# Kernel optimization log

Hardware: AMD Instinct MI355X
Metric: run time of the kernel (lower is better)

Reference implementation:

```python
import jax, jax.numpy as jnp
import numpy as np

B, S, E, L = 4, 4096, 64, 3
INIT_SCALE = 0.03


def setup_inputs() -> dict:
    key = jax.random.key(0)
    ks = jax.random.split(key, 7)
    return {
        "x": jax.random.normal(ks[0], (B, S, S + 1), dtype=jnp.float32),
        "q_ws": jax.random.normal(ks[1], (L, E, E), dtype=jnp.float32) * INIT_SCALE,
        "k_ws": jax.random.normal(ks[2], (L, E, E), dtype=jnp.float32) * INIT_SCALE,
        "v_ws": jax.random.normal(ks[3], (L, E, E), dtype=jnp.float32) * INIT_SCALE,
        "random_matrix": jax.random.normal(ks[4], (S, E - 1), dtype=jnp.float32) * INIT_SCALE,
        "coeffs_attended": jax.random.normal(ks[5], (S, E), dtype=jnp.float32) * INIT_SCALE,
        "offset": jax.random.normal(ks[6], (1,), dtype=jnp.float32),
    }


def reference(x, q_ws, k_ws, v_ws, random_matrix, coeffs_attended, offset):
    seq_length = random_matrix.shape[0]
    # project first seq_length feature columns, keep the last column raw -> [B, S, E]
    av = jnp.concatenate(
        [jnp.einsum('bsf,fe->bse', x[:, :, :seq_length], random_matrix), x[:, :, -1:]],
        axis=2,
    )

    def layer(av, ws):
        qw, kw, vw = ws
        q = jnp.einsum('bse,ed->bsd', av, qw)   # [B, S, E]
        k = jnp.einsum('bse,ed->bsd', av, kw)
        v = jnp.einsum('bse,ed->bsd', av, vw)
        scores = jax.nn.softmax(jnp.einsum('bqd,bkd->bqk', q, k), axis=-1)  # [B, S, S]
        out = jnp.einsum('bqk,bkd->bqd', scores, v)
        # skip_connections=False: output replaces attended values
        return out, None

    av, _ = jax.lax.scan(layer, av, (q_ws, k_ws, v_ws))
    final = jnp.einsum('bij,ij->b', av, coeffs_attended)  # [B]
    return final + offset[0]
```

## Files before the change

### kernel.cpp

```cpp
#include <hip/hip_runtime.h>

#define SEQ  4096
#define EMB  64
#define NB   4
#define XROW 4097

#define SW(r, c) ((r) * 64 + (((c) ^ ((r) & 7)) << 3))

typedef unsigned short ushort_t;
typedef __attribute__((ext_vector_type(8))) short short8;
typedef __attribute__((ext_vector_type(4))) float floatx4;

union U8 { uint4 u; short8 s8; };

__device__ __forceinline__ ushort_t f2bf(float f) {
    union { float f; unsigned int u; } v; v.f = f;
    unsigned int r = v.u + 0x7FFFu + ((v.u >> 16) & 1u);
    return (ushort_t)(r >> 16);
}
__device__ __forceinline__ uint2 pack4bf(float a, float b, float c, float d) {
    uint2 p;
    p.x = (unsigned)f2bf(a) | ((unsigned)f2bf(b) << 16);
    p.y = (unsigned)f2bf(c) | ((unsigned)f2bf(d) << 16);
    return p;
}

__global__ __launch_bounds__(256) void prep_rmt(const float* __restrict__ rm,
                                                ushort_t* __restrict__ rmT,
                                                float* __restrict__ out,
                                                const float* __restrict__ offset) {
    if (blockIdx.x == 0 && threadIdx.x < NB) out[threadIdx.x] = offset[0];
    int o = (blockIdx.x * 256 + threadIdx.x) * 4;
    int e = o >> 12;
    int f = o & 4095;
    alignas(8) ushort_t t[4];
    t[0] = f2bf((e < 63) ? rm[(size_t)(f + 0) * 63 + e] : 0.f);
    t[1] = f2bf((e < 63) ? rm[(size_t)(f + 1) * 63 + e] : 0.f);
    t[2] = f2bf((e < 63) ? rm[(size_t)(f + 2) * 63 + e] : 0.f);
    t[3] = f2bf((e < 63) ? rm[(size_t)(f + 3) * 63 + e] : 0.f);
    *(uint2*)&rmT[o] = *(uint2*)t;
}

__global__ __launch_bounds__(512) void proj_mfma(const float* __restrict__ x,
        const ushort_t* __restrict__ rmT, float* __restrict__ av) {
    __shared__ ushort_t xs[2][64 * 64];
    __shared__ ushort_t rs[2][64 * 64];
    const int tid = threadIdx.x;
    const int row0 = blockIdx.x * 64;
    const int w = tid >> 6, l = tid & 63;
    const int wg = w >> 2;
    const int wq = w & 3;
    const int t4 = tid & 255;
    const int srow = t4 >> 2, sc = (t4 & 3) * 16;
    const int c0 = (t4 & 3) * 2;
    const int kbase = wg * 2048;
    const int quad = l >> 4, q16 = l & 15;

    floatx4 acc[4];
    #pragma unroll
    for (int i = 0; i < 4; ++i) acc[i] = (floatx4){0.f, 0.f, 0.f, 0.f};

    float px[16];
    short8 pr0, pr1;
    {
        const float* xp = x + (size_t)(row0 + srow) * XROW + kbase + sc;
        #pragma unroll
        for (int i = 0; i < 16; ++i) px[i] = xp[i];
        const ushort_t* rp = rmT + (size_t)srow * SEQ + kbase + sc;
        pr0 = *(const short8*)&rp[0];
        pr1 = *(const short8*)&rp[8];
    }

    for (int k0 = 0; k0 < 2048; k0 += 64) {
        __syncthreads();
        {
            alignas(16) ushort_t tmp[16];
            #pragma unroll
            for (int i = 0; i < 16; ++i) tmp[i] = f2bf(px[i]);
            *(short8*)&xs[wg][SW(srow, c0)]     = *(short8*)&tmp[0];
            *(short8*)&xs[wg][SW(srow, c0 + 1)] = *(short8*)&tmp[8];
            *(short8*)&rs[wg][SW(srow, c0)]     = pr0;
            *(short8*)&rs[wg][SW(srow, c0 + 1)] = pr1;
        }
        __syncthreads();
        if (k0 + 64 < 2048) {
            const float* xp = x + (size_t)(row0 + srow) * XROW + kbase + k0 + 64 + sc;
            #pragma unroll
            for (int i = 0; i < 16; ++i) px[i] = xp[i];
            const ushort_t* rp = rmT + (size_t)srow * SEQ + kbase + k0 + 64 + sc;
            pr0 = *(const short8*)&rp[0];
            pr1 = *(const short8*)&rp[8];
        }
        #pragma unroll
        for (int ksp = 0; ksp < 2; ++ksp) {
            short8 a = *(short8*)&xs[wg][SW(wq * 16 + q16, ksp * 4 + quad)];
            #pragma unroll
            for (int nt = 0; nt < 4; ++nt) {
                short8 bf = *(short8*)&rs[wg][SW(nt * 16 + q16, ksp * 4 + quad)];
                acc[nt] = __builtin_amdgcn_mfma_f32_16x16x32_bf16(a, bf, acc[nt], 0, 0, 0);
            }
        }
    }

    __syncthreads();
    float* poc = (float*)xs;
    if (wg == 1) {
        #pragma unroll
        for (int nt = 0; nt < 4; ++nt)
            #pragma unroll
            for (int r = 0; r < 4; ++r)
                poc[(wq * 16 + quad * 4 + r) * 64 + nt * 16 + q16] = acc[nt][r];
    }
    __syncthreads();
    if (wg == 0) {
        #pragma unroll
        for (int nt = 0; nt < 4; ++nt)
            #pragma unroll
            for (int r = 0; r < 4; ++r) {
                int row = row0 + wq * 16 + quad * 4 + r;
                int col = nt * 16 + q16;
                float v = acc[nt][r] + poc[(wq * 16 + quad * 4 + r) * 64 + col];
                if (col == 63) v = x[(size_t)row * XROW + SEQ];
                av[(size_t)row * EMB + col] = v;
            }
    }
}

__global__ __launch_bounds__(256) void qkv_mfma(const float* __restrict__ av,
        const float* __restrict__ qw, const float* __restrict__ kw,
        const float* __restrict__ vw, ushort_t* __restrict__ Qb,
        ushort_t* __restrict__ Kb, ushort_t* __restrict__ Vt) {
    __shared__ ushort_t avs[64 * 64];
    __shared__ ushort_t wqs[64 * 64], wks[64 * 64], wvs[64 * 64];
    const int tid = threadIdx.x;
    const int row0 = blockIdx.x * 64;
    const int w = tid >> 6, l = tid & 63;
    const int srow = tid >> 2, sc = (tid & 3) * 16;
    const int c0 = (tid & 3) * 2;

    {
        const float* ap = av + (size_t)(row0 + srow) * EMB + sc;
        alignas(16) ushort_t tmp[16];
        #pragma unroll
        for (int i = 0; i < 16; ++i) tmp[i] = f2bf(ap[i]);
        *(short8*)&avs[SW(srow, c0)]     = *(short8*)&tmp[0];
        *(short8*)&avs[SW(srow, c0 + 1)] = *(short8*)&tmp[8];
    }
    {
        alignas(16) ushort_t tq[16], tk[16], tv[16];
        #pragma unroll
        for (int i = 0; i < 16; ++i) {
            int kk = sc + i;
            tq[i] = f2bf(qw[kk * 64 + srow]);
            tk[i] = f2bf(kw[kk * 64 + srow]);
            tv[i] = f2bf(vw[kk * 64 + srow]);
        }
        *(short8*)&wqs[SW(srow, c0)]     = *(short8*)&tq[0];
        *(short8*)&wqs[SW(srow, c0 + 1)] = *(short8*)&tq[8];
        *(short8*)&wks[SW(srow, c0)]     = *(short8*)&tk[0];
        *(short8*)&wks[SW(srow, c0 + 1)] = *(short8*)&tk[8];
        *(short8*)&wvs[SW(srow, c0)]     = *(short8*)&tv[0];
        *(short8*)&wvs[SW(srow, c0 + 1)] = *(short8*)&tv[8];
    }
    __syncthreads();

    floatx4 aq[4], ak[4], avv[4];
    #pragma unroll
    for (int i = 0; i < 4; ++i) {
        aq[i] = (floatx4){0.f, 0.f, 0.f, 0.f};
        ak[i] = aq[i]; avv[i] = aq[i];
    }
    #pragma unroll
    for (int ksp = 0; ksp < 2; ++ksp) {
        short8 a = *(short8*)&avs[SW(w * 16 + (l & 15), ksp * 4 + (l >> 4))];
        #pragma unroll
        for (int nt = 0; nt < 4; ++nt) {
            int bo = SW(nt * 16 + (l & 15), ksp * 4 + (l >> 4));
            aq[nt]  = __builtin_amdgcn_mfma_f32_16x16x32_bf16(a, *(short8*)&wqs[bo], aq[nt], 0, 0, 0);
            ak[nt]  = __builtin_amdgcn_mfma_f32_16x16x32_bf16(a, *(short8*)&wks[bo], ak[nt], 0, 0, 0);
            avv[nt] = __builtin_amdgcn_mfma_f32_16x16x32_bf16(a, *(short8*)&wvs[bo], avv[nt], 0, 0, 0);
        }
    }

    const int b = row0 >> 12;
    #pragma unroll
    for (int nt = 0; nt < 4; ++nt)
        #pragma unroll
        for (int r = 0; r < 4; ++r) {
            int row = row0 + w * 16 + (l >> 4) * 4 + r;
            int col = nt * 16 + (l & 15);
            size_t o = (size_t)row * EMB + col;
            Qb[o] = f2bf(aq[nt][r]);
            Kb[o] = f2bf(ak[nt][r]);
            Vt[((size_t)b * EMB + col) * SEQ + (row & 4095)] = f2bf(avv[nt][r]);
        }
}

__global__ __launch_bounds__(512) void flash_mfma(const ushort_t* __restrict__ Qb,
        const ushort_t* __restrict__ Kb, const ushort_t* __restrict__ Vt,
        float* __restrict__ out) {
    __shared__ ushort_t ks[2][64 * 64];
    __shared__ ushort_t vt[2][64 * 64];
    __shared__ ushort_t psbuf[8 * 1024];
    __shared__ float lrow[2][64];
    const int tid = threadIdx.x;
    const int w = tid >> 6, l = tid & 63;
    const int wg = w >> 2, wq = w & 3;
    const int quad = l >> 4, q16 = l & 15;
    const int b = blockIdx.y;
    const int q0 = blockIdx.x * 64;
    const size_t base  = (size_t)b * SEQ * EMB;
    const size_t vbase = (size_t)b * EMB * SEQ;
    const int t4 = tid & 255;
    const int srow = t4 >> 2, sc = (t4 & 3) * 16;
    const int c0 = (t4 & 3) * 2;
    const int kbase = wg * 2048;
    ushort_t* ps = &psbuf[w * 1024];

    short8 qf[2];
    #pragma unroll
    for (int ksp = 0; ksp < 2; ++ksp)
        qf[ksp] = *(const short8*)&Qb[base + (size_t)(q0 + wq * 16 + q16) * EMB
                                      + ksp * 32 + quad * 8];

    short8 pk0, pk1, pv0, pv1;
    {
        const ushort_t* kp = Kb + base + (size_t)(kbase + srow) * EMB + sc;
        pk0 = *(const short8*)kp;
        pk1 = *(const short8*)(kp + 8);
        const ushort_t* vp = Vt + vbase + (size_t)srow * SEQ + kbase + sc;
        pv0 = *(const short8*)vp;
        pv1 = *(const short8*)(vp + 8);
    }

    floatx4 o_acc[4];
    #pragma unroll
    for (int i = 0; i < 4; ++i) o_acc[i] = (floatx4){0.f, 0.f, 0.f, 0.f};
    float lpart = 0.f;

    for (int kt0 = 0; kt0 < 2048; kt0 += 64) {
        __syncthreads();
        *(short8*)&ks[wg][SW(srow, c0)]     = pk0;
        *(short8*)&ks[wg][SW(srow, c0 + 1)] = pk1;
        *(short8*)&vt[wg][SW(srow, c0)]     = pv0;
        *(short8*)&vt[wg][SW(srow, c0 + 1)] = pv1;
        __syncthreads();
        if (kt0 + 64 < 2048) {
            const ushort_t* kp = Kb + base + (size_t)(kbase + kt0 + 64 + srow) * EMB + sc;
            pk0 = *(const short8*)kp;
            pk1 = *(const short8*)(kp + 8);
            const ushort_t* vp = Vt + vbase + (size_t)srow * SEQ + kbase + kt0 + 64 + sc;
            pv0 = *(const short8*)vp;
            pv1 = *(const short8*)(vp + 8);
        }

        floatx4 s[4];
        #pragma unroll
        for (int nt = 0; nt < 4; ++nt) s[nt] = (floatx4){0.f, 0.f, 0.f, 0.f};
        #pragma unroll
        for (int ksp = 0; ksp < 2; ++ksp)
            #pragma unroll
            for (int nt = 0; nt < 4; ++nt) {
                short8 a = *(short8*)&ks[wg][SW(nt * 16 + q16, ksp * 4 + quad)];
                s[nt] = __builtin_amdgcn_mfma_f32_16x16x32_bf16(a, qf[ksp], s[nt], 0, 0, 0);
            }

        #pragma unroll
        for (int nt = 0; nt < 4; ++nt) {
            float p0 = __expf(s[nt][0]);
            float p1 = __expf(s[nt][1]);
            float p2 = __expf(s[nt][2]);
            float p3 = __expf(s[nt][3]);
            lpart += (p0 + p1) + (p2 + p3);
            int g = nt * 4 + quad;
            *(uint2*)&ps[q16 * 64 + ((g ^ q16) & 15) * 4] = pack4bf(p0, p1, p2, p3);
        }
        asm volatile("s_waitcnt lgkmcnt(0)" ::: "memory");

        #pragma unroll
        for (int ksp = 0; ksp < 2; ++ksp) {
            int g0 = ksp * 8 + quad * 2;
            uint2 a0 = *(uint2*)&ps[q16 * 64 + ((g0 ^ q16) & 15) * 4];
            uint2 a1 = *(uint2*)&ps[q16 * 64 + (((g0 + 1) ^ q16) & 15) * 4];
            U8 af;
            af.u.x = a0.x; af.u.y = a0.y; af.u.z = a1.x; af.u.w = a1.y;
            #pragma unroll
            for (int nt = 0; nt < 4; ++nt) {
                short8 bf = *(short8*)&vt[wg][SW(nt * 16 + q16, ksp * 4 + quad)];
                o_acc[nt] = __builtin_amdgcn_mfma_f32_16x16x32_bf16(af.s8, bf, o_acc[nt], 0, 0, 0);
            }
        }
    }

    lpart += __shfl_xor(lpart, 16);
    lpart += __shfl_xor(lpart, 32);
    __syncthreads();
    if (quad == 0) lrow[wg][wq * 16 + q16] = lpart;
    float* oc = (float*)psbuf;
    if (wg == 1) {
        #pragma unroll
        for (int nt = 0; nt < 4; ++nt)
            #pragma unroll
            for (int r = 0; r < 4; ++r)
                oc[(wq * 16 + quad * 4 + r) * 64 + nt * 16 + q16] = o_acc[nt][r];
    }
    __syncthreads();
    if (wg == 0) {
        float linv[4];
        #pragma unroll
        for (int r = 0; r < 4; ++r) {
            int q = wq * 16 + quad * 4 + r;
            linv[r] = 1.f / (lrow[0][q] + lrow[1][q]);
        }
        #pragma unroll
        for (int nt = 0; nt < 4; ++nt)
            #pragma unroll
            for (int r = 0; r < 4; ++r) {
                int row = q0 + wq * 16 + quad * 4 + r;
                int col = nt * 16 + q16;
                float v = (o_acc[nt][r] + oc[(wq * 16 + quad * 4 + r) * 64 + col]) * linv[r];
                out[base + (size_t)row * EMB + col] = v;
            }
    }
}

__global__ __launch_bounds__(256) void reduce_kernel(const float* __restrict__ av,
        const float* __restrict__ coeffs, float* __restrict__ out) {
    const int b = blockIdx.y;
    const size_t base = (size_t)b * SEQ * EMB;
    const int local0 = blockIdx.x * 4096;
    const int tid = threadIdx.x;
    float ssum = 0.f;
    #pragma unroll
    for (int i = 0; i < 4; ++i) {
        int idx = local0 + (tid + i * 256) * 4;
        float4 a = *(const float4*)&av[base + idx];
        float4 c = *(const float4*)&coeffs[idx];
        ssum += a.x * c.x + a.y * c.y + a.z * c.z + a.w * c.w;
    }
    #pragma unroll
    for (int off = 1; off < 64; off <<= 1) ssum += __shfl_xor(ssum, off);
    __shared__ float wsum[4];
    if ((tid & 63) == 0) wsum[tid >> 6] = ssum;
    __syncthreads();
    if (tid == 0)
        atomicAdd(&out[b], wsum[0] + wsum[1] + wsum[2] + wsum[3]);
}

extern "C" void kernel_launch(void* const* d_in, const int* in_sizes, int n_in,
                              void* d_out, int out_size, void* d_ws, size_t ws_size,
                              hipStream_t stream) {
    const float* x      = (const float*)d_in[0];
    const float* q_ws   = (const float*)d_in[1];
    const float* k_ws   = (const float*)d_in[2];
    const float* v_ws   = (const float*)d_in[3];
    const float* rm     = (const float*)d_in[4];
    const float* coeffs = (const float*)d_in[5];
    const float* offset = (const float*)d_in[6];
    float* out = (float*)d_out;
    char* ws = (char*)d_ws;

    float*    AV  = (float*)ws;
    ushort_t* Qb  = (ushort_t*)(ws + 4 * 1024 * 1024);
    ushort_t* Kb  = (ushort_t*)(ws + 6 * 1024 * 1024);
    ushort_t* Vt  = (ushort_t*)(ws + 8 * 1024 * 1024);
    ushort_t* rmT = (ushort_t*)(ws + 10 * 1024 * 1024);

    prep_rmt<<<256, 256, 0, stream>>>(rm, rmT, out, offset);
    proj_mfma<<<256, 512, 0, stream>>>(x, rmT, AV);
    for (int layer = 0; layer < 3; ++layer) {
        qkv_mfma<<<256, 256, 0, stream>>>(AV, q_ws + layer * 4096,
                                          k_ws + layer * 4096, v_ws + layer * 4096,
                                          Qb, Kb, Vt);
        flash_mfma<<<dim3(64, NB), 512, 0, stream>>>(Qb, Kb, Vt, AV);
    }
    reduce_kernel<<<dim3(64, NB), 256, 0, stream>>>(AV, coeffs, out);
}
```

Before: 531.8 us.

## Restructure flash kernel: 4-way key split, 32 query rows per wave, direct global K/V loads

The flash attention kernel now splits keys four ways across wave groups instead of two, and each wave handles 32 query rows so every K fragment feeds two MFMAs. K and V fragments are read straight from global memory (L2) into registers, which removes the shared-memory staging and the barriers inside the loop. A remapped block index spreads batches across XCDs. The cost is more global traffic per wave, higher register pressure, and a larger shared-memory reduction of four partial outputs at the end.

New measurement: 593.8 us. 11.7% more time.

```diff
diff --git a/kernel.cpp b/kernel.cpp
--- a/kernel.cpp
+++ b/kernel.cpp
@@ -199,128 +199,144 @@
 __global__ __launch_bounds__(512) void flash_mfma(const ushort_t* __restrict__ Qb,
         const ushort_t* __restrict__ Kb, const ushort_t* __restrict__ Vt,
         float* __restrict__ out) {
-    __shared__ ushort_t ks[2][64 * 64];
-    __shared__ ushort_t vt[2][64 * 64];
-    __shared__ ushort_t psbuf[8 * 1024];
-    __shared__ float lrow[2][64];
+    __shared__ ushort_t psbuf[8 * 2048];
+    __shared__ float comb[3][64 * 64];
+    __shared__ float lrow[4][64];
     const int tid = threadIdx.x;
     const int w = tid >> 6, l = tid & 63;
-    const int wg = w >> 2, wq = w & 3;
+    const int wg = w >> 1;
+    const int wq = w & 1;
     const int quad = l >> 4, q16 = l & 15;
-    const int b = blockIdx.y;
-    const int q0 = blockIdx.x * 64;
+    const int id2 = (blockIdx.x & 7) * 32 + (blockIdx.x >> 3);
+    const int b = id2 >> 6;
+    const int q0 = (id2 & 63) * 64;
     const size_t base  = (size_t)b * SEQ * EMB;
     const size_t vbase = (size_t)b * EMB * SEQ;
-    const int t4 = tid & 255;
-    const int srow = t4 >> 2, sc = (t4 & 3) * 16;
-    const int c0 = (t4 & 3) * 2;
-    const int kbase = wg * 2048;
-    ushort_t* ps = &psbuf[w * 1024];
-
-    short8 qf[2];
-    #pragma unroll
-    for (int ksp = 0; ksp < 2; ++ksp)
-        qf[ksp] = *(const short8*)&Qb[base + (size_t)(q0 + wq * 16 + q16) * EMB
-                                      + ksp * 32 + quad * 8];
-
-    short8 pk0, pk1, pv0, pv1;
-    {
-        const ushort_t* kp = Kb + base + (size_t)(kbase + srow) * EMB + sc;
-        pk0 = *(const short8*)kp;
-        pk1 = *(const short8*)(kp + 8);
-        const ushort_t* vp = Vt + vbase + (size_t)srow * SEQ + kbase + sc;
-        pv0 = *(const short8*)vp;
-        pv1 = *(const short8*)(vp + 8);
-    }
-
-    floatx4 o_acc[4];
-    #pragma unroll
-    for (int i = 0; i < 4; ++i) o_acc[i] = (floatx4){0.f, 0.f, 0.f, 0.f};
-    float lpart = 0.f;
-
-    for (int kt0 = 0; kt0 < 2048; kt0 += 64) {
-        __syncthreads();
-        *(short8*)&ks[wg][SW(srow, c0)]     = pk0;
-        *(short8*)&ks[wg][SW(srow, c0 + 1)] = pk1;
-        *(short8*)&vt[wg][SW(srow, c0)]     = pv0;
-        *(short8*)&vt[wg][SW(srow, c0 + 1)] = pv1;
-        __syncthreads();
-        if (kt0 + 64 < 2048) {
-            const ushort_t* kp = Kb + base + (size_t)(kbase + kt0 + 64 + srow) * EMB + sc;
-            pk0 = *(const short8*)kp;
-            pk1 = *(const short8*)(kp + 8);
-            const ushort_t* vp = Vt + vbase + (size_t)srow * SEQ + kbase + kt0 + 64 + sc;
-            pv0 = *(const short8*)vp;
-            pv1 = *(const short8*)(vp + 8);
-        }
-
-        floatx4 s[4];
-        #pragma unroll
-        for (int nt = 0; nt < 4; ++nt) s[nt] = (floatx4){0.f, 0.f, 0.f, 0.f};
+    const int kbase = wg * 1024;
+    ushort_t* ps = &psbuf[w * 2048];
+
+    short8 qf[2][2];
+    #pragma unroll
+    for (int qh = 0; qh < 2; ++qh)
         #pragma unroll
         for (int ksp = 0; ksp < 2; ++ksp)
+            qf[qh][ksp] = *(const short8*)&Qb[base
+                + (size_t)(q0 + wq * 32 + qh * 16 + q16) * EMB + ksp * 32 + quad * 8];
+
+    floatx4 o_acc[2][4];
+    #pragma unroll
+    for (int qh = 0; qh < 2; ++qh)
+        #pragma unroll
+        for (int i = 0; i < 4; ++i) o_acc[qh][i] = (floatx4){0.f, 0.f, 0.f, 0.f};
+    float lp0 = 0.f, lp1 = 0.f;
+
+    for (int kt0 = 0; kt0 < 1024; kt0 += 64) {
+        const int kt = kbase + kt0;
+
+        floatx4 s[2][4];
+        #pragma unroll
+        for (int qh = 0; qh < 2; ++qh)
+            #pragma unroll
+            for (int nt = 0; nt < 4; ++nt) s[qh][nt] = (floatx4){0.f, 0.f, 0.f, 0.f};
+        #pragma unroll
+        for (int ksp = 0; ksp < 2; ++ksp) {
+            short8 akf[4];
+            #pragma unroll
+            for (int nt = 0; nt < 4; ++nt)
+                akf[nt] = *(const short8*)&Kb[base
+                    + (size_t)(kt + nt * 16 + q16) * EMB + ksp * 32 + quad * 8];
             #pragma unroll
             for (int nt = 0; nt < 4; ++nt) {
-                short8 a = *(short8*)&ks[wg][SW(nt * 16 + q16, ksp * 4 + quad)];
-                s[nt] = __builtin_amdgcn_mfma_f32_16x16x32_bf16(a, qf[ksp], s[nt], 0, 0, 0);
-            }
+                s[0][nt] = __builtin_amdgcn_mfma_f32_16x16x32_bf16(akf[nt], qf[0][ksp], s[0][nt], 0, 0, 0);
+                s[1][nt] = __builtin_amdgcn_mfma_f32_16x16x32_bf16(akf[nt], qf[1][ksp], s[1][nt], 0, 0, 0);
+            }
+        }
+
+        short8 bv[2][4];
+        #pragma unroll
+        for (int ksp = 0; ksp < 2; ++ksp)
+            #pragma unroll
+            for (int nt = 0; nt < 4; ++nt)
+                bv[ksp][nt] = *(const short8*)&Vt[vbase
+                    + (size_t)(nt * 16 + q16) * SEQ + kt + ksp * 32 + quad * 8];
 
         #pragma unroll
         for (int nt = 0; nt < 4; ++nt) {
-            float p0 = __expf(s[nt][0]);
-            float p1 = __expf(s[nt][1]);
-            float p2 = __expf(s[nt][2]);
-            float p3 = __expf(s[nt][3]);
-            lpart += (p0 + p1) + (p2 + p3);
+            float p0 = __expf(s[0][nt][0]);
+            float p1 = __expf(s[0][nt][1]);
+            float p2 = __expf(s[0][nt][2]);
+            float p3 = __expf(s[0][nt][3]);
+            lp0 += (p0 + p1) + (p2 + p3);
             int g = nt * 4 + quad;
             *(uint2*)&ps[q16 * 64 + ((g ^ q16) & 15) * 4] = pack4bf(p0, p1, p2, p3);
         }
+        #pragma unroll
+        for (int nt = 0; nt < 4; ++nt) {
+            float p0 = __expf(s[1][nt][0]);
+            float p1 = __expf(s[1][nt][1]);
+            float p2 = __expf(s[1][nt][2]);
+            float p3 = __expf(s[1][nt][3]);
+            lp1 += (p0 + p1) + (p2 + p3);
+            int g = nt * 4 + quad;
+            *(uint2*)&ps[1024 + q16 * 64 + ((g ^ q16) & 15) * 4] = pack4bf(p0, p1, p2, p3);
+        }
         asm volatile("s_waitcnt lgkmcnt(0)" ::: "memory");
 
         #pragma unroll
         for (int ksp = 0; ksp < 2; ++ksp) {
-            int g0 = ksp * 8 + quad * 2;
-            uint2 a0 = *(uint2*)&ps[q16 * 64 + ((g0 ^ q16) & 15) * 4];
-            uint2 a1 = *(uint2*)&ps[q16 * 64 + (((g0 + 1) ^ q16) & 15) * 4];
-            U8 af;
-            af.u.x = a0.x; af.u.y = a0.y; af.u.z = a1.x; af.u.w = a1.y;
-            #pragma unroll
-            for (int nt = 0; nt < 4; ++nt) {
-                short8 bf = *(short8*)&vt[wg][SW(nt * 16 + q16, ksp * 4 + quad)];
-                o_acc[nt] = __builtin_amdgcn_mfma_f32_16x16x32_bf16(af.s8, bf, o_acc[nt], 0, 0, 0);
-            }
-        }
-    }
-
-    lpart += __shfl_xor(lpart, 16);
-    lpart += __shfl_xor(lpart, 32);
-    __syncthreads();
-    if (quad == 0) lrow[wg][wq * 16 + q16] = lpart;
-    float* oc = (float*)psbuf;
-    if (wg == 1) {
-        #pragma unroll
-        for (int nt = 0; nt < 4; ++nt)
-            #pragma unroll
-            for (int r = 0; r < 4; ++r)
-                oc[(wq * 16 + quad * 4 + r) * 64 + nt * 16 + q16] = o_acc[nt][r];
+            #pragma unroll
+            for (int qh = 0; qh < 2; ++qh) {
+                int g0 = ksp * 8 + quad * 2;
+                uint2 a0 = *(uint2*)&ps[qh * 1024 + q16 * 64 + ((g0 ^ q16) & 15) * 4];
+                uint2 a1 = *(uint2*)&ps[qh * 1024 + q16 * 64 + (((g0 + 1) ^ q16) & 15) * 4];
+                U8 af;
+                af.u.x = a0.x; af.u.y = a0.y; af.u.z = a1.x; af.u.w = a1.y;
+                #pragma unroll
+                for (int nt = 0; nt < 4; ++nt)
+                    o_acc[qh][nt] = __builtin_amdgcn_mfma_f32_16x16x32_bf16(af.s8, bv[ksp][nt], o_acc[qh][nt], 0, 0, 0);
+            }
+        }
+    }
+
+    lp0 += __shfl_xor(lp0, 16);
+    lp0 += __shfl_xor(lp0, 32);
+    lp1 += __shfl_xor(lp1, 16);
+    lp1 += __shfl_xor(lp1, 32);
+    if (quad == 0) {
+        lrow[wg][wq * 32 + q16]      = lp0;
+        lrow[wg][wq * 32 + 16 + q16] = lp1;
+    }
+    if (wg > 0) {
+        #pragma unroll
+        for (int qh = 0; qh < 2; ++qh)
+            #pragma unroll
+            for (int nt = 0; nt < 4; ++nt)
+                #pragma unroll
+                for (int r = 0; r < 4; ++r)
+                    comb[wg - 1][(wq * 32 + qh * 16 + quad * 4 + r) * 64 + nt * 16 + q16]
+                        = o_acc[qh][nt][r];
     }
     __syncthreads();
     if (wg == 0) {
-        float linv[4];
-        #pragma unroll
-        for (int r = 0; r < 4; ++r) {
-            int q = wq * 16 + quad * 4 + r;
-            linv[r] = 1.f / (lrow[0][q] + lrow[1][q]);
-        }
-        #pragma unroll
-        for (int nt = 0; nt < 4; ++nt)
+        #pragma unroll
+        for (int qh = 0; qh < 2; ++qh) {
+            float linv[4];
             #pragma unroll
             for (int r = 0; r < 4; ++r) {
-                int row = q0 + wq * 16 + quad * 4 + r;
-                int col = nt * 16 + q16;
-                float v = (o_acc[nt][r] + oc[(wq * 16 + quad * 4 + r) * 64 + col]) * linv[r];
-                out[base + (size_t)row * EMB + col] = v;
-            }
+                int ql = wq * 32 + qh * 16 + quad * 4 + r;
+                linv[r] = 1.f / (lrow[0][ql] + lrow[1][ql] + lrow[2][ql] + lrow[3][ql]);
+            }
+            #pragma unroll
+            for (int nt = 0; nt < 4; ++nt)
+                #pragma unroll
+                for (int r = 0; r < 4; ++r) {
+                    int ql = wq * 32 + qh * 16 + quad * 4 + r;
+                    int col = nt * 16 + q16;
+                    float v = (o_acc[qh][nt][r] + comb[0][ql * 64 + col]
+                               + comb[1][ql * 64 + col] + comb[2][ql * 64 + col]) * linv[r];
+                    out[base + (size_t)(q0 + ql) * EMB + col] = v;
+                }
+        }
     }
 }
 
@@ -372,7 +388,7 @@
         qkv_mfma<<<256, 256, 0, stream>>>(AV, q_ws + layer * 4096,
                                           k_ws + layer * 4096, v_ws + layer * 4096,
                                           Qb, Kb, Vt);
-        flash_mfma<<<dim3(64, NB), 512, 0, stream>>>(Qb, Kb, Vt, AV);
+        flash_mfma<<<256, 512, 0, stream>>>(Qb, Kb, Vt, AV);
     }
     reduce_kernel<<<dim3(64, NB), 256, 0, stream>>>(AV, coeffs, out);
 }
```
